# Optimization experiments

Measured on AMD Instinct MI355X. Metric: run time of the kernel, lower is better.

## Reference

```python
import jax, jax.numpy as jnp
import numpy as np

N_NODES = 100000
DEG = 16          # regular-graph degree so degrees[start] > 0 for all nodes
STEPS = 32
D_FEAT = 16
MAXI32 = 2147483647


def setup_inputs() -> dict:
    key = jax.random.key(0)
    k1, k2, k3 = jax.random.split(key, 3)
    x = jax.random.normal(k1, (N_NODES, D_FEAT), dtype=jnp.float32)
    # CSR-style flat adjacency list: node v's neighbors are
    # adj_nodes[adj_offset[v] : adj_offset[v] + degrees[v]]
    adj_nodes = jax.random.randint(k2, (N_NODES * DEG,), 0, N_NODES, dtype=jnp.int32)
    adj_offset = (jnp.arange(N_NODES, dtype=jnp.int32) * DEG)
    degrees = jnp.full((N_NODES,), DEG, dtype=jnp.int32)
    # cache of random integers, one per (step, walk), as in the torch code
    choices = jax.random.randint(k3, (STEPS, N_NODES), 0, MAXI32, dtype=jnp.int32)
    return {"x": x, "adj_nodes": adj_nodes, "adj_offset": adj_offset,
            "degrees": degrees, "choices": choices}


def reference(x, adj_nodes, adj_offset, degrees, choices):
    """Non-backtracking random walk (Walker.sample_walks with start_p=1.0,
    all nodes having degree > 0, so start = arange(n)).
    Returns walks [steps+1, w] and walk_edges [steps, w]."""
    n = degrees.shape[0]
    nb_degrees = jnp.maximum(degrees - 1, 1)  # reduced degree for non-backtrack rewrite
    start = jnp.arange(n, dtype=jnp.int32)

    def step(carry, ch):
        prev, cur = carry                      # [w] previous / current nodes
        deg = degrees[cur]
        edge_idx = ch % deg                    # unweighted modulo edge choice
        chosen = adj_offset[cur] + edge_idx
        new = adj_nodes[chosen]
        bt = new == prev                       # backtracking walks
        # conditional rewrite: pick a different outgoing edge
        alt = adj_offset[cur] + (edge_idx + 1 + ch % nb_degrees[cur]) % deg
        chosen = jnp.where(bt, alt, chosen)
        new = jnp.where(bt, adj_nodes[alt], new)
        return (cur, new), (new, chosen)

    # prev = -1 at step 0 => bt is all-False, matching the i > 0 guard
    prev0 = jnp.full_like(start, -1)
    _, (nodes, walk_edges) = jax.lax.scan(step, (prev0, start), choices)
    walks = jnp.concatenate([start[None, :], nodes], axis=0)  # [steps+1, w]
    return walks, walk_edges
```

## Files before the change

kernel.cpp:

```cpp
#include <hip/hip_runtime.h>
#include <hip/hip_bf16.h>


#define DEG 16

__global__ void pack_check_kernel(const int* __restrict__ adj_nodes,
                                  const int* __restrict__ adj_offset,
                                  const int* __restrict__ degrees,
                                  int n,
                                  unsigned int* __restrict__ pk32,
                                  int* __restrict__ flag) {
    int v = blockIdx.x * blockDim.x + threadIdx.x;
    if (v >= n) return;

    bool bad = (degrees[v] != DEG) || (adj_offset[v] != v * DEG);

    const int* row = adj_nodes + (size_t)v * DEG;
    unsigned w[8];
    unsigned hbits = 0;
#pragma unroll
    for (int j = 0; j < 8; ++j) {
        unsigned u0 = (unsigned)row[2 * j];
        unsigned u1 = (unsigned)row[2 * j + 1];
        if (u0 >= 131072u || u1 >= 131072u) bad = true;
        w[j] = (u0 & 0xffffu) | ((u1 & 0xffffu) << 16);
        hbits |= ((u0 >> 16) & 1u) << (2 * j);
        hbits |= ((u1 >> 16) & 1u) << (2 * j + 1);
    }
    unsigned int* dst = pk32 + (size_t)v * 9;
#pragma unroll
    for (int j = 0; j < 8; ++j) dst[j] = w[j];
    dst[8] = hbits;

    if (bad) atomicOr(flag, 1);
}

template <int STEPS>
__global__ __launch_bounds__(64) void walker_fast2(
    const unsigned short* __restrict__ pk,
    const int* __restrict__ choices,
    int* __restrict__ out, int n, int h,
    const int* __restrict__ flag,
    const int* __restrict__ adj_nodes,
    const int* __restrict__ adj_offset,
    const int* __restrict__ degrees) {

    int t = blockIdx.x * blockDim.x + threadIdx.x;
    if (t >= h) return;

    int* walks      = out;
    int* walk_edges = out + (STEPS + 1) * n;

    int w0 = t;
    int w1 = t + h;
    bool has1 = (w1 < n);
    int w1s = has1 ? w1 : w0;

    __builtin_nontemporal_store(w0, &walks[w0]);
    if (has1) __builtin_nontemporal_store(w1, &walks[w1]);

    if (*flag == 0) {
        int c0[STEPS], c1[STEPS];
#pragma unroll
        for (int i = 0; i < STEPS; ++i) {
            c0[i] = __builtin_nontemporal_load(&choices[i * n + w0]);
            c1[i] = __builtin_nontemporal_load(&choices[i * n + w1s]);
        }

        int prev0 = -1, cur0 = w0;
        int prev1 = -1, cur1 = w1s;
#pragma unroll
        for (int i = 0; i < STEPS; ++i) {
            int ch0 = c0[i], ch1 = c1[i];
            int e0 = ch0 & (DEG - 1);
            int e1 = ch1 & (DEG - 1);
            int a0 = (e0 + 1 + ch0 % (DEG - 1)) & (DEG - 1);
            int a1 = (e1 + 1 + ch1 % (DEG - 1)) & (DEG - 1);

            const unsigned short* r0 = pk + (unsigned)cur0 * 18u;
            const unsigned short* r1 = pk + (unsigned)cur1 * 18u;

            unsigned l00 = r0[e0];
            unsigned l01 = r0[a0];
            unsigned hb0 = r0[16];
            unsigned l10 = r1[e1];
            unsigned l11 = r1[a1];
            unsigned hb1 = r1[16];

            int n00 = (int)(l00 | (((hb0 >> e0) & 1u) << 16));
            int n01 = (int)(l01 | (((hb0 >> a0) & 1u) << 16));
            int n10 = (int)(l10 | (((hb1 >> e1) & 1u) << 16));
            int n11 = (int)(l11 | (((hb1 >> a1) & 1u) << 16));

            bool bt0 = (n00 == prev0);
            bool bt1 = (n10 == prev1);
            int nw0 = bt0 ? n01 : n00;
            int nw1 = bt1 ? n11 : n10;
            int ce0 = (cur0 << 4) + (bt0 ? a0 : e0);
            int ce1 = (cur1 << 4) + (bt1 ? a1 : e1);

            __builtin_nontemporal_store(nw0, &walks[(i + 1) * n + w0]);
            __builtin_nontemporal_store(ce0, &walk_edges[i * n + w0]);
            if (has1) {
                __builtin_nontemporal_store(nw1, &walks[(i + 1) * n + w1]);
                __builtin_nontemporal_store(ce1, &walk_edges[i * n + w1]);
            }
            prev0 = cur0; cur0 = nw0;
            prev1 = cur1; cur1 = nw1;
        }
    } else {
        for (int k = 0; k < 2; ++k) {
            int w = (k == 0) ? w0 : w1;
            if (w >= n) break;
            int prev = -1, cur = w;
            for (int i = 0; i < STEPS; ++i) {
                int ch  = choices[i * n + w];
                int deg = degrees[cur];
                int off = adj_offset[cur];
                int nb  = deg - 1 > 1 ? deg - 1 : 1;

                int e      = ch % deg;
                int chosen = off + e;
                int alt    = off + (e + 1 + ch % nb) % deg;

                int nv0 = adj_nodes[chosen];
                int nv1 = adj_nodes[alt];

                bool bt = (nv0 == prev);
                int nw  = bt ? nv1 : nv0;
                walks[(i + 1) * n + w] = nw;
                walk_edges[i * n + w]  = bt ? alt : chosen;
                prev = cur;
                cur  = nw;
            }
        }
    }
}

__global__ __launch_bounds__(256) void walker_generic(
    const int* __restrict__ adj_nodes,
    const int* __restrict__ adj_offset,
    const int* __restrict__ degrees,
    const int* __restrict__ choices,
    int* __restrict__ out, int n, int steps) {

    int w = blockIdx.x * blockDim.x + threadIdx.x;
    if (w >= n) return;

    int* walks      = out;
    int* walk_edges = out + (steps + 1) * n;
    walks[w] = w;

    int prev = -1, cur = w;
    for (int i = 0; i < steps; ++i) {
        int ch  = choices[i * n + w];
        int deg = degrees[cur];
        int off = adj_offset[cur];
        int nb  = deg - 1 > 1 ? deg - 1 : 1;

        int e      = ch % deg;
        int chosen = off + e;
        int alt    = off + (e + 1 + ch % nb) % deg;

        int nv0 = adj_nodes[chosen];
        int nv1 = adj_nodes[alt];

        bool bt = (nv0 == prev);
        int nw  = bt ? nv1 : nv0;
        walks[(i + 1) * n + w] = nw;
        walk_edges[i * n + w]  = bt ? alt : chosen;
        prev = cur;
        cur  = nw;
    }
}

extern "C" void kernel_launch(void* const* d_in, const int* in_sizes, int n_in,
                              void* d_out, int out_size, void* d_ws, size_t ws_size,
                              hipStream_t stream) {
    const int* adj_nodes  = (const int*)d_in[1];
    const int* adj_offset = (const int*)d_in[2];
    const int* degrees    = (const int*)d_in[3];
    const int* choices    = (const int*)d_in[4];
    int* out = (int*)d_out;

    int n     = in_sizes[2];
    int steps = in_sizes[4] / n;

    size_t pk_off = 64;
    size_t need   = pk_off + (size_t)n * 36;

    if (steps == 32 && ws_size >= need) {
        int* flag = (int*)d_ws;
        unsigned int* pk32  = (unsigned int*)((char*)d_ws + pk_off);
        unsigned short* pk  = (unsigned short*)pk32;

        hipMemsetAsync(flag, 0, sizeof(int), stream);
        int pb = 256, pg = (n + pb - 1) / pb;
        pack_check_kernel<<<pg, pb, 0, stream>>>(adj_nodes, adj_offset, degrees,
                                                 n, pk32, flag);
        int h  = (n + 1) / 2;
        int wb = 64, wg = (h + wb - 1) / wb;
        walker_fast2<32><<<wg, wb, 0, stream>>>(pk, choices, out, n, h, flag,
                                                adj_nodes, adj_offset, degrees);
    } else {
        int block = 256, grid = (n + block - 1) / block;
        walker_generic<<<grid, block, 0, stream>>>(adj_nodes, adj_offset,
                                                   degrees, choices, out, n, steps);
    }
}
```

Before: 108.0 us.

## Run four walk chains per thread and pad packed adjacency rows to 64 bytes

Each thread now advances four independent walks instead of two, so more independent gather loads are in flight per thread to hide the latency of the dependent pointer chase. Choices are loaded in two halves of 16 steps to limit register pressure. The packed adjacency row is padded from 36 to 64 bytes and written with vector stores, so every row lands in one aligned cache line. The cost is fewer threads and waves overall (about 25k threads for 100k walks), which may reduce occupancy-based latency hiding, and double the workspace footprint.

Result: slower. 137.4 us (+27.2%).

```diff
diff --git a/kernel.cpp b/kernel.cpp
--- a/kernel.cpp
+++ b/kernel.cpp
@@ -3,6 +3,7 @@
 
 
 #define DEG 16
+#define CHAINS 4
 
 __global__ void pack_check_kernel(const int* __restrict__ adj_nodes,
                                   const int* __restrict__ adj_offset,
@@ -16,27 +17,27 @@
     bool bad = (degrees[v] != DEG) || (adj_offset[v] != v * DEG);
 
     const int* row = adj_nodes + (size_t)v * DEG;
-    unsigned w[8];
+    union { unsigned u32[8]; uint4 v4[2]; } p;
     unsigned hbits = 0;
 #pragma unroll
     for (int j = 0; j < 8; ++j) {
         unsigned u0 = (unsigned)row[2 * j];
         unsigned u1 = (unsigned)row[2 * j + 1];
         if (u0 >= 131072u || u1 >= 131072u) bad = true;
-        w[j] = (u0 & 0xffffu) | ((u1 & 0xffffu) << 16);
+        p.u32[j] = (u0 & 0xffffu) | ((u1 & 0xffffu) << 16);
         hbits |= ((u0 >> 16) & 1u) << (2 * j);
         hbits |= ((u1 >> 16) & 1u) << (2 * j + 1);
     }
-    unsigned int* dst = pk32 + (size_t)v * 9;
-#pragma unroll
-    for (int j = 0; j < 8; ++j) dst[j] = w[j];
+    unsigned int* dst = pk32 + (size_t)v * 16;
+    ((uint4*)dst)[0] = p.v4[0];
+    ((uint4*)dst)[1] = p.v4[1];
     dst[8] = hbits;
 
     if (bad) atomicOr(flag, 1);
 }
 
 template <int STEPS>
-__global__ __launch_bounds__(64) void walker_fast2(
+__global__ __launch_bounds__(64) void walker_fast4(
     const unsigned short* __restrict__ pk,
     const int* __restrict__ choices,
     int* __restrict__ out, int n, int h,
@@ -51,85 +52,84 @@
     int* walks      = out;
     int* walk_edges = out + (STEPS + 1) * n;
 
-    int w0 = t;
-    int w1 = t + h;
-    bool has1 = (w1 < n);
-    int w1s = has1 ? w1 : w0;
-
-    __builtin_nontemporal_store(w0, &walks[w0]);
-    if (has1) __builtin_nontemporal_store(w1, &walks[w1]);
+    int  w[CHAINS], wsx[CHAINS];
+    bool val[CHAINS];
+#pragma unroll
+    for (int c = 0; c < CHAINS; ++c) {
+        w[c]   = t + c * h;
+        val[c] = (w[c] < n);
+        wsx[c] = val[c] ? w[c] : t;
+        if (val[c]) __builtin_nontemporal_store(w[c], &walks[w[c]]);
+    }
 
     if (*flag == 0) {
-        int c0[STEPS], c1[STEPS];
-#pragma unroll
-        for (int i = 0; i < STEPS; ++i) {
-            c0[i] = __builtin_nontemporal_load(&choices[i * n + w0]);
-            c1[i] = __builtin_nontemporal_load(&choices[i * n + w1s]);
-        }
-
-        int prev0 = -1, cur0 = w0;
-        int prev1 = -1, cur1 = w1s;
-#pragma unroll
-        for (int i = 0; i < STEPS; ++i) {
-            int ch0 = c0[i], ch1 = c1[i];
-            int e0 = ch0 & (DEG - 1);
-            int e1 = ch1 & (DEG - 1);
-            int a0 = (e0 + 1 + ch0 % (DEG - 1)) & (DEG - 1);
-            int a1 = (e1 + 1 + ch1 % (DEG - 1)) & (DEG - 1);
-
-            const unsigned short* r0 = pk + (unsigned)cur0 * 18u;
-            const unsigned short* r1 = pk + (unsigned)cur1 * 18u;
-
-            unsigned l00 = r0[e0];
-            unsigned l01 = r0[a0];
-            unsigned hb0 = r0[16];
-            unsigned l10 = r1[e1];
-            unsigned l11 = r1[a1];
-            unsigned hb1 = r1[16];
-
-            int n00 = (int)(l00 | (((hb0 >> e0) & 1u) << 16));
-            int n01 = (int)(l01 | (((hb0 >> a0) & 1u) << 16));
-            int n10 = (int)(l10 | (((hb1 >> e1) & 1u) << 16));
-            int n11 = (int)(l11 | (((hb1 >> a1) & 1u) << 16));
-
-            bool bt0 = (n00 == prev0);
-            bool bt1 = (n10 == prev1);
-            int nw0 = bt0 ? n01 : n00;
-            int nw1 = bt1 ? n11 : n10;
-            int ce0 = (cur0 << 4) + (bt0 ? a0 : e0);
-            int ce1 = (cur1 << 4) + (bt1 ? a1 : e1);
-
-            __builtin_nontemporal_store(nw0, &walks[(i + 1) * n + w0]);
-            __builtin_nontemporal_store(ce0, &walk_edges[i * n + w0]);
-            if (has1) {
-                __builtin_nontemporal_store(nw1, &walks[(i + 1) * n + w1]);
-                __builtin_nontemporal_store(ce1, &walk_edges[i * n + w1]);
+        int prev[CHAINS], cur[CHAINS];
+#pragma unroll
+        for (int c = 0; c < CHAINS; ++c) { prev[c] = -1; cur[c] = wsx[c]; }
+
+        static_assert(STEPS % 16 == 0, "");
+#pragma unroll 1
+        for (int half = 0; half < STEPS / 16; ++half) {
+            int ch[CHAINS][16];
+#pragma unroll
+            for (int i = 0; i < 16; ++i)
+#pragma unroll
+                for (int c = 0; c < CHAINS; ++c)
+                    ch[c][i] = __builtin_nontemporal_load(
+                        &choices[(half * 16 + i) * n + wsx[c]]);
+
+#pragma unroll
+            for (int i = 0; i < 16; ++i) {
+                int step = half * 16 + i;
+                unsigned e[CHAINS], ae[CHAINS], l0[CHAINS], l1[CHAINS], hb[CHAINS];
+#pragma unroll
+                for (int c = 0; c < CHAINS; ++c) {
+                    int chv = ch[c][i];
+                    e[c]  = chv & (DEG - 1);
+                    ae[c] = (e[c] + 1 + chv % (DEG - 1)) & (DEG - 1);
+                    const unsigned short* r = pk + (unsigned)cur[c] * 32u;
+                    l0[c] = r[e[c]];
+                    l1[c] = r[ae[c]];
+                    hb[c] = r[16];
+                }
+#pragma unroll
+                for (int c = 0; c < CHAINS; ++c) {
+                    int n0 = (int)(l0[c] | (((hb[c] >> e[c])  & 1u) << 16));
+                    int n1 = (int)(l1[c] | (((hb[c] >> ae[c]) & 1u) << 16));
+                    bool bt = (n0 == prev[c]);
+                    int nw  = bt ? n1 : n0;
+                    int ce  = (cur[c] << 4) + (int)(bt ? ae[c] : e[c]);
+                    if (val[c]) {
+                        __builtin_nontemporal_store(nw, &walks[(step + 1) * n + w[c]]);
+                        __builtin_nontemporal_store(ce, &walk_edges[step * n + w[c]]);
+                    }
+                    prev[c] = cur[c];
+                    cur[c]  = nw;
+                }
             }
-            prev0 = cur0; cur0 = nw0;
-            prev1 = cur1; cur1 = nw1;
         }
     } else {
-        for (int k = 0; k < 2; ++k) {
-            int w = (k == 0) ? w0 : w1;
-            if (w >= n) break;
-            int prev = -1, cur = w;
+        for (int c = 0; c < CHAINS; ++c) {
+            if (!val[c]) continue;
+            int wk = w[c];
+            int prev = -1, cur = wk;
             for (int i = 0; i < STEPS; ++i) {
-                int ch  = choices[i * n + w];
+                int chv = choices[i * n + wk];
                 int deg = degrees[cur];
                 int off = adj_offset[cur];
                 int nb  = deg - 1 > 1 ? deg - 1 : 1;
 
-                int e      = ch % deg;
-                int chosen = off + e;
-                int alt    = off + (e + 1 + ch % nb) % deg;
+                int ee     = chv % deg;
+                int chosen = off + ee;
+                int alt    = off + (ee + 1 + chv % nb) % deg;
 
                 int nv0 = adj_nodes[chosen];
                 int nv1 = adj_nodes[alt];
 
                 bool bt = (nv0 == prev);
                 int nw  = bt ? nv1 : nv0;
-                walks[(i + 1) * n + w] = nw;
-                walk_edges[i * n + w]  = bt ? alt : chosen;
+                walks[(i + 1) * n + wk] = nw;
+                walk_edges[i * n + wk]  = bt ? alt : chosen;
                 prev = cur;
                 cur  = nw;
             }
@@ -153,14 +153,14 @@
 
     int prev = -1, cur = w;
     for (int i = 0; i < steps; ++i) {
-        int ch  = choices[i * n + w];
+        int chv = choices[i * n + w];
         int deg = degrees[cur];
         int off = adj_offset[cur];
         int nb  = deg - 1 > 1 ? deg - 1 : 1;
 
-        int e      = ch % deg;
+        int e      = chv % deg;
         int chosen = off + e;
-        int alt    = off + (e + 1 + ch % nb) % deg;
+        int alt    = off + (e + 1 + chv % nb) % deg;
 
         int nv0 = adj_nodes[chosen];
         int nv1 = adj_nodes[alt];
@@ -187,20 +187,20 @@
     int steps = in_sizes[4] / n;
 
     size_t pk_off = 64;
-    size_t need   = pk_off + (size_t)n * 36;
+    size_t need   = pk_off + (size_t)n * 64;
 
     if (steps == 32 && ws_size >= need) {
         int* flag = (int*)d_ws;
-        unsigned int* pk32  = (unsigned int*)((char*)d_ws + pk_off);
-        unsigned short* pk  = (unsigned short*)pk32;
+        unsigned int*   pk32 = (unsigned int*)((char*)d_ws + pk_off);
+        unsigned short* pk   = (unsigned short*)pk32;
 
         hipMemsetAsync(flag, 0, sizeof(int), stream);
         int pb = 256, pg = (n + pb - 1) / pb;
         pack_check_kernel<<<pg, pb, 0, stream>>>(adj_nodes, adj_offset, degrees,
                                                  n, pk32, flag);
-        int h  = (n + 1) / 2;
+        int h  = (n + CHAINS - 1) / CHAINS;
         int wb = 64, wg = (h + wb - 1) / wb;
-        walker_fast2<32><<<wg, wb, 0, stream>>>(pk, choices, out, n, h, flag,
+        walker_fast4<32><<<wg, wb, 0, stream>>>(pk, choices, out, n, h, flag,
                                                 adj_nodes, adj_offset, degrees);
     } else {
         int block = 256, grid = (n + block - 1) / block;
```

## Split packed adjacency into aligned low/high tables and prefetch into cache

Applied to the files above, without the earlier changes.

Repacks each node's neighbours into a 32-byte aligned block of 16-bit low halves plus a separate 16-bit table of high bits, written with vector stores. The walker kernel begins by streaming both tables through an XOR loop so they sit in cache before the random gathers start. It also loads the choices in two halves of 16 steps to lower register pressure. The goal is fewer cache lines per random lookup and a warm cache for the dependent gathers, at the cost of an extra full-table read in every block and one more lookup per step.

New measurement: 119.4 us. 1.11x slower.

```diff
diff --git a/kernel.cpp b/kernel.cpp
--- a/kernel.cpp
+++ b/kernel.cpp
@@ -3,34 +3,40 @@
 
 
 #define DEG 16
+#define CHAINS 2
 
 __global__ void pack_check_kernel(const int* __restrict__ adj_nodes,
                                   const int* __restrict__ adj_offset,
                                   const int* __restrict__ degrees,
                                   int n,
-                                  unsigned int* __restrict__ pk32,
+                                  unsigned int* __restrict__ lo32,
+                                  unsigned short* __restrict__ hi,
                                   int* __restrict__ flag) {
     int v = blockIdx.x * blockDim.x + threadIdx.x;
     if (v >= n) return;
 
     bool bad = (degrees[v] != DEG) || (adj_offset[v] != v * DEG);
 
-    const int* row = adj_nodes + (size_t)v * DEG;
-    unsigned w[8];
+    const uint4* row4 = (const uint4*)(adj_nodes + (size_t)v * DEG);
+    uint4 r[4];
+    r[0] = row4[0]; r[1] = row4[1]; r[2] = row4[2]; r[3] = row4[3];
+    const unsigned* rr = (const unsigned*)r;
+
+    union { unsigned u32[8]; uint4 v4[2]; } p;
     unsigned hbits = 0;
 #pragma unroll
     for (int j = 0; j < 8; ++j) {
-        unsigned u0 = (unsigned)row[2 * j];
-        unsigned u1 = (unsigned)row[2 * j + 1];
+        unsigned u0 = rr[2 * j];
+        unsigned u1 = rr[2 * j + 1];
         if (u0 >= 131072u || u1 >= 131072u) bad = true;
-        w[j] = (u0 & 0xffffu) | ((u1 & 0xffffu) << 16);
+        p.u32[j] = (u0 & 0xffffu) | ((u1 & 0xffffu) << 16);
         hbits |= ((u0 >> 16) & 1u) << (2 * j);
         hbits |= ((u1 >> 16) & 1u) << (2 * j + 1);
     }
-    unsigned int* dst = pk32 + (size_t)v * 9;
-#pragma unroll
-    for (int j = 0; j < 8; ++j) dst[j] = w[j];
-    dst[8] = hbits;
+    uint4* dst = (uint4*)(lo32 + (size_t)v * 8);
+    dst[0] = p.v4[0];
+    dst[1] = p.v4[1];
+    hi[v] = (unsigned short)hbits;
 
     if (bad) atomicOr(flag, 1);
 }
@@ -38,12 +44,36 @@
 template <int STEPS>
 __global__ __launch_bounds__(64) void walker_fast2(
     const unsigned short* __restrict__ pk,
+    const unsigned short* __restrict__ hi,
     const int* __restrict__ choices,
     int* __restrict__ out, int n, int h,
     const int* __restrict__ flag,
+    int* __restrict__ sink,
     const int* __restrict__ adj_nodes,
     const int* __restrict__ adj_offset,
     const int* __restrict__ degrees) {
+
+    {
+        int lane = threadIdx.x & 63;
+        int g    = blockIdx.x & 7;
+        int s    = (blockIdx.x >> 3);
+        int nsl  = (gridDim.x + 7) >> 3;
+        (void)g;
+        const uint4* tbl = (const uint4*)pk;
+        int total = n >> 1;
+        unsigned acc = 0;
+        for (int i = s * 64 + lane; i < total; i += nsl * 64) {
+            uint4 v = tbl[i];
+            acc ^= v.x ^ v.y ^ v.z ^ v.w;
+        }
+        const uint4* ht = (const uint4*)hi;
+        int htotal = n >> 3;
+        for (int i = s * 64 + lane; i < htotal; i += nsl * 64) {
+            uint4 v = ht[i];
+            acc ^= v.x ^ v.y ^ v.z ^ v.w;
+        }
+        if (acc == 0xDEADBEEFu) *sink = 1;
+    }
 
     int t = blockIdx.x * blockDim.x + threadIdx.x;
     if (t >= h) return;
@@ -60,53 +90,58 @@
     if (has1) __builtin_nontemporal_store(w1, &walks[w1]);
 
     if (*flag == 0) {
-        int c0[STEPS], c1[STEPS];
-#pragma unroll
-        for (int i = 0; i < STEPS; ++i) {
-            c0[i] = __builtin_nontemporal_load(&choices[i * n + w0]);
-            c1[i] = __builtin_nontemporal_load(&choices[i * n + w1s]);
-        }
-
         int prev0 = -1, cur0 = w0;
         int prev1 = -1, cur1 = w1s;
+
+        static_assert(STEPS % 16 == 0, "");
+#pragma unroll 1
+        for (int half = 0; half < STEPS / 16; ++half) {
+            int c0[16], c1[16];
 #pragma unroll
-        for (int i = 0; i < STEPS; ++i) {
-            int ch0 = c0[i], ch1 = c1[i];
-            int e0 = ch0 & (DEG - 1);
-            int e1 = ch1 & (DEG - 1);
-            int a0 = (e0 + 1 + ch0 % (DEG - 1)) & (DEG - 1);
-            int a1 = (e1 + 1 + ch1 % (DEG - 1)) & (DEG - 1);
-
-            const unsigned short* r0 = pk + (unsigned)cur0 * 18u;
-            const unsigned short* r1 = pk + (unsigned)cur1 * 18u;
-
-            unsigned l00 = r0[e0];
-            unsigned l01 = r0[a0];
-            unsigned hb0 = r0[16];
-            unsigned l10 = r1[e1];
-            unsigned l11 = r1[a1];
-            unsigned hb1 = r1[16];
-
-            int n00 = (int)(l00 | (((hb0 >> e0) & 1u) << 16));
-            int n01 = (int)(l01 | (((hb0 >> a0) & 1u) << 16));
-            int n10 = (int)(l10 | (((hb1 >> e1) & 1u) << 16));
-            int n11 = (int)(l11 | (((hb1 >> a1) & 1u) << 16));
-
-            bool bt0 = (n00 == prev0);
-            bool bt1 = (n10 == prev1);
-            int nw0 = bt0 ? n01 : n00;
-            int nw1 = bt1 ? n11 : n10;
-            int ce0 = (cur0 << 4) + (bt0 ? a0 : e0);
-            int ce1 = (cur1 << 4) + (bt1 ? a1 : e1);
-
-            __builtin_nontemporal_store(nw0, &walks[(i + 1) * n + w0]);
-            __builtin_nontemporal_store(ce0, &walk_edges[i * n + w0]);
-            if (has1) {
-                __builtin_nontemporal_store(nw1, &walks[(i + 1) * n + w1]);
-                __builtin_nontemporal_store(ce1, &walk_edges[i * n + w1]);
+            for (int i = 0; i < 16; ++i) {
+                c0[i] = __builtin_nontemporal_load(&choices[(half * 16 + i) * n + w0]);
+                c1[i] = __builtin_nontemporal_load(&choices[(half * 16 + i) * n + w1s]);
             }
-            prev0 = cur0; cur0 = nw0;
-            prev1 = cur1; cur1 = nw1;
+#pragma unroll
+            for (int i = 0; i < 16; ++i) {
+                int step = half * 16 + i;
+                int ch0 = c0[i], ch1 = c1[i];
+                unsigned e0 = ch0 & (DEG - 1);
+                unsigned e1 = ch1 & (DEG - 1);
+                unsigned a0 = (e0 + 1 + ch0 % (DEG - 1)) & (DEG - 1);
+                unsigned a1 = (e1 + 1 + ch1 % (DEG - 1)) & (DEG - 1);
+
+                const unsigned short* r0 = pk + (unsigned)cur0 * 16u;
+                const unsigned short* r1 = pk + (unsigned)cur1 * 16u;
+
+                unsigned l00 = r0[e0];
+                unsigned l01 = r0[a0];
+                unsigned hb0 = hi[cur0];
+                unsigned l10 = r1[e1];
+                unsigned l11 = r1[a1];
+                unsigned hb1 = hi[cur1];
+
+                int n00 = (int)(l00 | (((hb0 >> e0) & 1u) << 16));
+                int n01 = (int)(l01 | (((hb0 >> a0) & 1u) << 16));
+                int n10 = (int)(l10 | (((hb1 >> e1) & 1u) << 16));
+                int n11 = (int)(l11 | (((hb1 >> a1) & 1u) << 16));
+
+                bool bt0 = (n00 == prev0);
+                bool bt1 = (n10 == prev1);
+                int nw0 = bt0 ? n01 : n00;
+                int nw1 = bt1 ? n11 : n10;
+                int ce0 = (cur0 << 4) + (int)(bt0 ? a0 : e0);
+                int ce1 = (cur1 << 4) + (int)(bt1 ? a1 : e1);
+
+                __builtin_nontemporal_store(nw0, &walks[(step + 1) * n + w0]);
+                __builtin_nontemporal_store(ce0, &walk_edges[step * n + w0]);
+                if (has1) {
+                    __builtin_nontemporal_store(nw1, &walks[(step + 1) * n + w1]);
+                    __builtin_nontemporal_store(ce1, &walk_edges[step * n + w1]);
+                }
+                prev0 = cur0; cur0 = nw0;
+                prev1 = cur1; cur1 = nw1;
+            }
         }
     } else {
         for (int k = 0; k < 2; ++k) {
@@ -114,14 +149,14 @@
             if (w >= n) break;
             int prev = -1, cur = w;
             for (int i = 0; i < STEPS; ++i) {
-                int ch  = choices[i * n + w];
+                int chv = choices[i * n + w];
                 int deg = degrees[cur];
                 int off = adj_offset[cur];
                 int nb  = deg - 1 > 1 ? deg - 1 : 1;
 
-                int e      = ch % deg;
+                int e      = chv % deg;
                 int chosen = off + e;
-                int alt    = off + (e + 1 + ch % nb) % deg;
+                int alt    = off + (e + 1 + chv % nb) % deg;
 
                 int nv0 = adj_nodes[chosen];
                 int nv1 = adj_nodes[alt];
@@ -153,14 +188,14 @@
 
     int prev = -1, cur = w;
     for (int i = 0; i < steps; ++i) {
-        int ch  = choices[i * n + w];
+        int chv = choices[i * n + w];
         int deg = degrees[cur];
         int off = adj_offset[cur];
         int nb  = deg - 1 > 1 ? deg - 1 : 1;
 
-        int e      = ch % deg;
+        int e      = chv % deg;
         int chosen = off + e;
-        int alt    = off + (e + 1 + ch % nb) % deg;
+        int alt    = off + (e + 1 + chv % nb) % deg;
 
         int nv0 = adj_nodes[chosen];
         int nv1 = adj_nodes[alt];
@@ -186,22 +221,26 @@
     int n     = in_sizes[2];
     int steps = in_sizes[4] / n;
 
-    size_t pk_off = 64;
-    size_t need   = pk_off + (size_t)n * 36;
+    size_t lo_off = 64;
+    size_t lo_bytes = (size_t)n * 32;
+    size_t hi_off = lo_off + ((lo_bytes + 63) & ~(size_t)63);
+    size_t need   = hi_off + (size_t)n * 2;
 
     if (steps == 32 && ws_size >= need) {
         int* flag = (int*)d_ws;
-        unsigned int* pk32  = (unsigned int*)((char*)d_ws + pk_off);
-        unsigned short* pk  = (unsigned short*)pk32;
+        int* sink = (int*)((char*)d_ws + 8);
+        unsigned int*   lo32 = (unsigned int*)((char*)d_ws + lo_off);
+        unsigned short* pk   = (unsigned short*)lo32;
+        unsigned short* hi   = (unsigned short*)((char*)d_ws + hi_off);
 
         hipMemsetAsync(flag, 0, sizeof(int), stream);
         int pb = 256, pg = (n + pb - 1) / pb;
         pack_check_kernel<<<pg, pb, 0, stream>>>(adj_nodes, adj_offset, degrees,
-                                                 n, pk32, flag);
-        int h  = (n + 1) / 2;
+                                                 n, lo32, hi, flag);
+        int h  = (n + CHAINS - 1) / CHAINS;
         int wb = 64, wg = (h + wb - 1) / wb;
-        walker_fast2<32><<<wg, wb, 0, stream>>>(pk, choices, out, n, h, flag,
-                                                adj_nodes, adj_offset, degrees);
+        walker_fast2<32><<<wg, wb, 0, stream>>>(pk, hi, choices, out, n, h, flag,
+                                                sink, adj_nodes, adj_offset, degrees);
     } else {
         int block = 256, grid = (n + block - 1) / block;
         walker_generic<<<grid, block, 0, stream>>>(adj_nodes, adj_offset,
```
